# Performance work log

Hardware: AMD Instinct MI355X
Metric: run time of the kernel (lower is better)

The kernel has to match this reference:

```python
import jax, jax.numpy as jnp
import numpy as np

COMMITMENT_COST = 0.25
N, D, K = 131072, 64, 1024


def setup_inputs() -> dict:
    key = jax.random.key(0)
    k1, k2 = jax.random.split(key)
    inputs = jax.random.normal(k1, (N, D), dtype=jnp.float32)
    # torch init: uniform(-1/K, 1/K)
    weight = jax.random.uniform(k2, (K, D), dtype=jnp.float32,
                                minval=-1.0 / K, maxval=1.0 / K)
    return {"inputs": inputs, "weight": weight}


def reference(inputs, weight):
    x2 = jnp.sum(inputs * inputs, axis=1, keepdims=True)          # [N, 1]
    e2 = jnp.sum(weight * weight, axis=1)                          # [K]
    distances = x2 + e2 - 2.0 * jnp.matmul(inputs, weight.T)       # [N, K]
    encoding_indices = jnp.argmin(distances, axis=1)               # [N]
    # scatter one-hot + matmul in the original == direct gather
    quantized = jnp.take(weight, encoding_indices, axis=0)         # [N, D]
    e_latent_loss = jnp.mean((jax.lax.stop_gradient(quantized) - inputs) ** 2)
    q_latent_loss = jnp.mean((quantized - jax.lax.stop_gradient(inputs)) ** 2)
    loss = q_latent_loss + COMMITMENT_COST * e_latent_loss
    # straight-through estimator
    quantized_st = inputs + jax.lax.stop_gradient(quantized - inputs)
    return (quantized_st, loss, encoding_indices)
```

## Files before the change

### kernel.cpp

```cpp
#include <hip/hip_runtime.h>


#define NROWS 131072
#define DIM 64
#define KCODES 1024
#define MARGIN 5e-5f
#define X2_GUARD 120.0f
#define LOSS_SCALE (1.25f / ((float)NROWS * (float)DIM))
#define PADID (1 << 20)

typedef short bf16x8 __attribute__((ext_vector_type(8)));
typedef float f32x4 __attribute__((ext_vector_type(4)));

__device__ __forceinline__ short f2bf(float f) {
    unsigned u = __float_as_uint(f);
    u += 0x7FFF + ((u >> 16) & 1);
    return (short)(u >> 16);
}
__device__ __forceinline__ float bf2f(short h) {
    return __uint_as_float(((unsigned)(unsigned short)h) << 16);
}

__global__ __launch_bounds__(256) void prep_w(const float* __restrict__ w,
                                              float* __restrict__ e2,
                                              short* __restrict__ w_hi,
                                              short* __restrict__ w_lo,
                                              float* __restrict__ out_loss,
                                              unsigned* __restrict__ flag_cnt) {
    int k = blockIdx.x * blockDim.x + threadIdx.x;
    if (k == 0) { *out_loss = 0.0f; *flag_cnt = 0u; }
    if (k >= KCODES) return;
    const float* wk = w + (size_t)k * DIM;
    float r[DIM];
#pragma unroll
    for (int i = 0; i < DIM / 4; ++i) *(float4*)&r[4 * i] = *(const float4*)(wk + 4 * i);
    float s = 0.f;
#pragma unroll
    for (int d = 0; d < DIM; ++d) s = fmaf(r[d], r[d], s);
    e2[k] = s;

    const int t = k >> 5, ct = (k >> 4) & 1, m = k & 15;
#pragma unroll
    for (int kc = 0; kc < 2; ++kc)
#pragma unroll
        for (int q = 0; q < 4; ++q) {
            bf16x8 hv, lv;
#pragma unroll
            for (int j = 0; j < 8; ++j) {
                float f = -2.0f * r[kc * 32 + q * 8 + j];
                short h = f2bf(f);
                hv[j] = h;
                lv[j] = f2bf(f - bf2f(h));
            }
            size_t fo = ((size_t)(((t * 2 + ct) * 2 + kc) * 4 + q) * 16 + m) * 8;
            *(bf16x8*)(w_hi + fo) = hv;
            *(bf16x8*)(w_lo + fo) = lv;
        }
}

#define MINPAIR(av, ai, bv, bi)                                   \
    { bool tk_ = (bv < av) || (bv == av && bi < ai);              \
      av = tk_ ? bv : av; ai = tk_ ? bi : ai; }
#define CEX(xv, xi, yv, yi)                                       \
    { bool tk_ = (yv < xv) || (yv == xv && yi < xi);              \
      float tv_ = xv; int ti_ = xi;                               \
      xv = tk_ ? yv : xv; xi = tk_ ? yi : xi;                     \
      yv = tk_ ? tv_ : yv; yi = tk_ ? ti_ : yi; }

__global__ __launch_bounds__(256, 3) void vq_main(
        const float* __restrict__ x, const float* __restrict__ w,
        const float* __restrict__ e2,
        const short* __restrict__ w_hi, const short* __restrict__ w_lo,
        float* __restrict__ out_q, float* __restrict__ out_loss,
        float* __restrict__ out_idx,
        unsigned* __restrict__ flag_cnt, unsigned* __restrict__ flag_list) {
    const int tid = threadIdx.x;
    const int lane = tid & 63;
    const int wv = tid >> 6;
    const int m = lane & 15;
    const int q = lane >> 4;
    const int block_row0 = blockIdx.x * 128;
    const int wave_row0 = block_row0 + wv * 32;

    __shared__ int sidx[128];
    __shared__ int scnd[128][2];
    __shared__ unsigned char sflg[128];
    __shared__ float red[4];

    float xa[2][2][8];
#pragma unroll
    for (int rt = 0; rt < 2; ++rt) {
        const float* xr = x + (size_t)(wave_row0 + rt * 16 + m) * DIM + q * 8;
        *(float4*)&xa[rt][0][0] = *(const float4*)(xr);
        *(float4*)&xa[rt][0][4] = *(const float4*)(xr + 4);
        *(float4*)&xa[rt][1][0] = *(const float4*)(xr + 32);
        *(float4*)&xa[rt][1][4] = *(const float4*)(xr + 36);
    }
    bf16x8 ah[2][2], al[2][2];
#pragma unroll
    for (int rt = 0; rt < 2; ++rt)
#pragma unroll
        for (int c = 0; c < 2; ++c)
#pragma unroll
            for (int j = 0; j < 8; ++j) {
                float f = xa[rt][c][j];
                short h = f2bf(f);
                ah[rt][c][j] = h;
                al[rt][c][j] = f2bf(f - bf2f(h));
            }

    float best[2][4], sec[2][4];
    int bidx[2][4], sbix[2][4];
#pragma unroll
    for (int rt = 0; rt < 2; ++rt)
#pragma unroll
        for (int r = 0; r < 4; ++r) {
            best[rt][r] = 3.4e38f;
            sec[rt][r] = 3.4e38f;
            bidx[rt][r] = PADID;
            sbix[rt][r] = PADID;
        }

    const short* ph = w_hi + q * 128 + m * 8;
    const short* pl = w_lo + q * 128 + m * 8;
    const float* pe = e2 + m;

    for (int t = 0; t < KCODES / 32; ++t) {
        bf16x8 bh[2][2], bl[2][2];
#pragma unroll
        for (int ct = 0; ct < 2; ++ct)
#pragma unroll
            for (int kc = 0; kc < 2; ++kc) {
                int off = t * 2048 + (ct * 2 + kc) * 512;
                bh[ct][kc] = *(const bf16x8*)(ph + off);
                bl[ct][kc] = *(const bf16x8*)(pl + off);
            }
        float e2c0 = pe[t * 32];
        float e2c1 = pe[t * 32 + 16];

#pragma unroll
        for (int rt = 0; rt < 2; ++rt)
#pragma unroll
            for (int ct = 0; ct < 2; ++ct) {
                float ei = ct ? e2c1 : e2c0;
                f32x4 a = {ei, ei, ei, ei};
                a = __builtin_amdgcn_mfma_f32_16x16x32_bf16(al[rt][0], bh[ct][0], a, 0, 0, 0);
                a = __builtin_amdgcn_mfma_f32_16x16x32_bf16(ah[rt][0], bl[ct][0], a, 0, 0, 0);
                a = __builtin_amdgcn_mfma_f32_16x16x32_bf16(ah[rt][0], bh[ct][0], a, 0, 0, 0);
                a = __builtin_amdgcn_mfma_f32_16x16x32_bf16(al[rt][1], bh[ct][1], a, 0, 0, 0);
                a = __builtin_amdgcn_mfma_f32_16x16x32_bf16(ah[rt][1], bl[ct][1], a, 0, 0, 0);
                a = __builtin_amdgcn_mfma_f32_16x16x32_bf16(ah[rt][1], bh[ct][1], a, 0, 0, 0);
                int id = t * 32 + ct * 16 + m;
#pragma unroll
                for (int r = 0; r < 4; ++r) {
                    float g = a[r];
                    bool ltb = g < best[rt][r];
                    bool lts = g < sec[rt][r];
                    float nsec = ltb ? best[rt][r] : (lts ? g : sec[rt][r]);
                    int nsid = ltb ? bidx[rt][r] : (lts ? id : sbix[rt][r]);
                    best[rt][r] = ltb ? g : best[rt][r];
                    bidx[rt][r] = ltb ? id : bidx[rt][r];
                    sec[rt][r] = nsec;
                    sbix[rt][r] = nsid;
                }
            }
    }

    if (m == 0) {  }
#pragma unroll
    for (int rt = 0; rt < 2; ++rt)
#pragma unroll
        for (int r = 0; r < 4; ++r) {
            float v0 = best[rt][r], v1 = sec[rt][r], v2 = 3.4e38f, v3 = 3.4e38f;
            int j0 = bidx[rt][r], j1 = sbix[rt][r], j2 = PADID, j3 = PADID;
#pragma unroll
            for (int off = 1; off < 16; off <<= 1) {
                float b0 = __shfl_xor(v0, off, 64);
                float b1 = __shfl_xor(v1, off, 64);
                float b2 = __shfl_xor(v2, off, 64);
                float b3 = __shfl_xor(v3, off, 64);
                int k0 = __shfl_xor(j0, off, 64);
                int k1 = __shfl_xor(j1, off, 64);
                int k2 = __shfl_xor(j2, off, 64);
                int k3 = __shfl_xor(j3, off, 64);
                MINPAIR(v0, j0, b3, k3);
                MINPAIR(v1, j1, b2, k2);
                MINPAIR(v2, j2, b1, k1);
                MINPAIR(v3, j3, b0, k0);
                CEX(v0, j0, v2, j2);
                CEX(v1, j1, v3, j3);
                CEX(v0, j0, v1, j1);
                CEX(v2, j2, v3, j3);
            }
            if (m == 0) {
                bool w1 = v1 < v0 + MARGIN;
                bool w2 = v2 < v0 + MARGIN;
                bool w3 = v3 < v0 + MARGIN;
                bool samem = (w1 && ((j0 & 15) == (j1 & 15))) ||
                             (w2 && (((j0 & 15) == (j2 & 15)) ||
                                     ((j1 & 15) == (j2 & 15))));
                int meta;
                if (w3 || samem) meta = 3;
                else if (w2) meta = 2;
                else if (w1) meta = 1;
                else meta = 0;
                int lr = wv * 32 + rt * 16 + q * 4 + r;
                sidx[lr] = j0;
                scnd[lr][0] = j1;
                scnd[lr][1] = j2;
                sflg[lr] = (unsigned char)meta;
                if (meta == 3) {
                    unsigned p = atomicAdd(flag_cnt, 1u);
                    flag_list[p] = (unsigned)(block_row0 + lr);
                }
            }
        }
    __syncthreads();

    float lsum = 0.f;
    const int rl = tid >> 2, part = tid & 3;
#pragma unroll
    for (int p = 0; p < 2; ++p) {
        int lr = p * 64 + rl;
        int grow = block_row0 + lr;
        int meta = sflg[lr];
        if (meta == 0) {
            int bi = sidx[lr];
            const float* xs = x + (size_t)grow * DIM + part * 16;
            const float* ws = w + (size_t)bi * DIM + part * 16;
            float* os = out_q + (size_t)grow * DIM + part * 16;
#pragma unroll
            for (int i = 0; i < 4; ++i) {
                float4 xv = *(const float4*)(xs + 4 * i);
                float4 wv4 = *(const float4*)(ws + 4 * i);
                float d0 = wv4.x - xv.x, d1 = wv4.y - xv.y;
                float d2 = wv4.z - xv.z, d3 = wv4.w - xv.w;
                lsum = fmaf(d0, d0, lsum);
                lsum = fmaf(d1, d1, lsum);
                lsum = fmaf(d2, d2, lsum);
                lsum = fmaf(d3, d3, lsum);
                float4 o = {xv.x + d0, xv.y + d1, xv.z + d2, xv.w + d3};
                *(float4*)(os + 4 * i) = o;
            }
            if (part == 0) out_idx[grow] = (float)bi;
        } else if (meta != 3) {
            int nc = meta + 1;
            int cand = (part == 0) ? sidx[lr]
                     : (part == 1) ? scnd[lr][0] : scnd[lr][1];
            unsigned long long key = ~0ULL;
            float x2v = 0.f;
            if (part < nc) {
                const float* xr = x + (size_t)grow * DIM;
                const float* wr = w + (size_t)cand * DIM;
                float dot = 0.f;
#pragma unroll
                for (int d4 = 0; d4 < 16; ++d4) {
                    float4 xv = *(const float4*)(xr + 4 * d4);
                    float4 wv4 = *(const float4*)(wr + 4 * d4);
                    x2v = fmaf(xv.x, xv.x, x2v);
                    x2v = fmaf(xv.y, xv.y, x2v);
                    x2v = fmaf(xv.z, xv.z, x2v);
                    x2v = fmaf(xv.w, xv.w, x2v);
                    dot = fmaf(xv.x, wv4.x, dot);
                    dot = fmaf(xv.y, wv4.y, dot);
                    dot = fmaf(xv.z, wv4.z, dot);
                    dot = fmaf(xv.w, wv4.w, dot);
                }
                float dist = (x2v + e2[cand]) - 2.0f * dot;
                key = ((unsigned long long)__float_as_uint(dist) << 32) |
                      (unsigned)cand;
            }
            {
                unsigned long long o1 = __shfl_xor(key, 1, 64);
                key = key < o1 ? key : o1;
                unsigned long long o2 = __shfl_xor(key, 2, 64);
                key = key < o2 ? key : o2;
            }
            float x2b = __shfl(x2v, lane & 60, 64);
            if (x2b >= X2_GUARD) {
                if (part == 0) {
                    unsigned pp = atomicAdd(flag_cnt, 1u);
                    flag_list[pp] = (unsigned)grow;
                }
            } else {
                int bi = (int)(unsigned)(key & 0xFFFFFFFFu);
                const float* xs = x + (size_t)grow * DIM + part * 16;
                const float* ws = w + (size_t)bi * DIM + part * 16;
                float* os = out_q + (size_t)grow * DIM + part * 16;
#pragma unroll
                for (int i = 0; i < 4; ++i) {
                    float4 xv = *(const float4*)(xs + 4 * i);
                    float4 wv4 = *(const float4*)(ws + 4 * i);
                    float d0 = wv4.x - xv.x, d1 = wv4.y - xv.y;
                    float d2 = wv4.z - xv.z, d3 = wv4.w - xv.w;
                    lsum = fmaf(d0, d0, lsum);
                    lsum = fmaf(d1, d1, lsum);
                    lsum = fmaf(d2, d2, lsum);
                    lsum = fmaf(d3, d3, lsum);
                    float4 o = {xv.x + d0, xv.y + d1, xv.z + d2, xv.w + d3};
                    *(float4*)(os + 4 * i) = o;
                }
                if (part == 0) out_idx[grow] = (float)bi;
            }
        }
    }

    for (int off = 32; off > 0; off >>= 1) lsum += __shfl_down(lsum, off, 64);
    if ((tid & 63) == 0) red[tid >> 6] = lsum;
    __syncthreads();
    if (tid == 0) {
        float s = (red[0] + red[1]) + (red[2] + red[3]);
        atomicAdd(out_loss, s * LOSS_SCALE);
    }
}

#define CH 16
__global__ __launch_bounds__(256) void vq_cleanup(
        const float* __restrict__ x, const float* __restrict__ w,
        const float* __restrict__ e2,
        const unsigned* __restrict__ flag_cnt,
        const unsigned* __restrict__ flag_list,
        float* __restrict__ out_q, float* __restrict__ out_loss,
        float* __restrict__ out_idx) {
    __shared__ float xs[CH][68];
    __shared__ float wt[128][68];
    __shared__ float sx2[CH];
    const int tid = threadIdx.x;
    const int rowsub = tid >> 4;
    const int kslot = tid & 15;
    const unsigned cnt = *flag_cnt;

    for (unsigned base = blockIdx.x * CH; base < cnt; base += gridDim.x * CH) {
        const int nrows = (int)min((unsigned)CH, cnt - base);
        __syncthreads();
        {
            int rr = tid >> 4, sg = tid & 15;
            if (rr < nrows) {
                unsigned grow = flag_list[base + rr];
                *(float4*)&xs[rr][sg * 4] =
                    *(const float4*)(x + (size_t)grow * DIM + sg * 4);
            }
        }
        __syncthreads();
        if (tid < nrows) {
            float s = 0.f;
#pragma unroll
            for (int d = 0; d < DIM; ++d) s = fmaf(xs[tid][d], xs[tid][d], s);
            sx2[tid] = s;
        }

        unsigned long long kmin = ~0ULL;
        for (int tile = 0; tile < KCODES / 128; ++tile) {
            __syncthreads();
#pragma unroll
            for (int i = 0; i < 8; ++i) {
                int f = tid + i * 256;
                int code = f >> 4, sg = f & 15;
                *(float4*)&wt[code][sg * 4] =
                    *(const float4*)(w + (size_t)(tile * 128 + code) * DIM + sg * 4);
            }
            __syncthreads();
            if (rowsub < nrows) {
#pragma unroll
                for (int j = 0; j < 8; ++j) {
                    int cl = j * 16 + kslot;
                    int code = tile * 128 + cl;
                    float dot = 0.f;
#pragma unroll
                    for (int d4 = 0; d4 < 16; ++d4) {
                        float4 wv4 = *(const float4*)&wt[cl][d4 * 4];
                        float4 xv4 = *(const float4*)&xs[rowsub][d4 * 4];
                        dot = fmaf(wv4.x, xv4.x, dot);
                        dot = fmaf(wv4.y, xv4.y, dot);
                        dot = fmaf(wv4.z, xv4.z, dot);
                        dot = fmaf(wv4.w, xv4.w, dot);
                    }
                    float dist = (sx2[rowsub] + e2[code]) - 2.0f * dot;
                    unsigned long long key =
                        ((unsigned long long)__float_as_uint(dist) << 32) |
                        (unsigned)code;
                    kmin = kmin < key ? kmin : key;
                }
            }
        }
#pragma unroll
        for (int off = 1; off < 16; off <<= 1) {
            unsigned long long o = __shfl_xor(kmin, off, 64);
            kmin = kmin < o ? kmin : o;
        }
        if (rowsub < nrows) {
            int bi = (int)(unsigned)(kmin & 0xFFFFFFFFu);
            unsigned grow = flag_list[base + rowsub];
            float4 x4 = *(float4*)&xs[rowsub][kslot * 4];
            float4 w4 = *(const float4*)(w + (size_t)bi * DIM + kslot * 4);
            float d0 = w4.x - x4.x, d1 = w4.y - x4.y;
            float d2 = w4.z - x4.z, d3 = w4.w - x4.w;
            float ls = 0.f;
            ls = fmaf(d0, d0, ls);
            ls = fmaf(d1, d1, ls);
            ls = fmaf(d2, d2, ls);
            ls = fmaf(d3, d3, ls);
            float4 o = {x4.x + d0, x4.y + d1, x4.z + d2, x4.w + d3};
            *(float4*)(out_q + (size_t)grow * DIM + kslot * 4) = o;
            if (kslot == 0) out_idx[grow] = (float)bi;
#pragma unroll
            for (int off = 1; off < 16; off <<= 1)
                ls += __shfl_xor(ls, off, 64);
            if (kslot == 0) atomicAdd(out_loss, ls * LOSS_SCALE);
        }
    }
}

extern "C" void kernel_launch(void* const* d_in, const int* in_sizes, int n_in,
                              void* d_out, int out_size, void* d_ws, size_t ws_size,
                              hipStream_t stream) {
    const float* x = (const float*)d_in[0];
    const float* w = (const float*)d_in[1];

    float* out_q    = (float*)d_out;
    float* out_loss = (float*)d_out + (size_t)NROWS * DIM;
    float* out_idx  = out_loss + 1;

    float* e2 = (float*)d_ws;
    short* w_hi = (short*)(e2 + KCODES);
    short* w_lo = w_hi + (size_t)KCODES * DIM;
    unsigned* cnt = (unsigned*)(w_lo + (size_t)KCODES * DIM);
    unsigned* list = cnt + 1;

    prep_w<<<(KCODES + 255) / 256, 256, 0, stream>>>(w, e2, w_hi, w_lo,
                                                     out_loss, cnt);
    vq_main<<<NROWS / 128, 256, 0, stream>>>(x, w, e2, w_hi, w_lo,
                                             out_q, out_loss, out_idx, cnt, list);
    vq_cleanup<<<256, 256, 0, stream>>>(x, w, e2, cnt, list,
                                        out_q, out_loss, out_idx);
}
```

Before: 202.6 us.

## Fuse fallback exact-search into main kernel using per-block shared flag list

```diff
diff --git a/kernel.cpp b/kernel.cpp
--- a/kernel.cpp
+++ b/kernel.cpp
@@ -25,10 +25,9 @@
                                               float* __restrict__ e2,
                                               short* __restrict__ w_hi,
                                               short* __restrict__ w_lo,
-                                              float* __restrict__ out_loss,
-                                              unsigned* __restrict__ flag_cnt) {
+                                              float* __restrict__ out_loss) {
     int k = blockIdx.x * blockDim.x + threadIdx.x;
-    if (k == 0) { *out_loss = 0.0f; *flag_cnt = 0u; }
+    if (k == 0) *out_loss = 0.0f;
     if (k >= KCODES) return;
     const float* wk = w + (size_t)k * DIM;
     float r[DIM];
@@ -72,8 +71,7 @@
         const float* __restrict__ e2,
         const short* __restrict__ w_hi, const short* __restrict__ w_lo,
         float* __restrict__ out_q, float* __restrict__ out_loss,
-        float* __restrict__ out_idx,
-        unsigned* __restrict__ flag_cnt, unsigned* __restrict__ flag_list) {
+        float* __restrict__ out_idx) {
     const int tid = threadIdx.x;
     const int lane = tid & 63;
     const int wv = tid >> 6;
@@ -86,6 +84,10 @@
     __shared__ int scnd[128][2];
     __shared__ unsigned char sflg[128];
     __shared__ float red[4];
+    __shared__ int hcnt;
+    __shared__ short hlist[128];
+
+    if (tid == 0) hcnt = 0;
 
     float xa[2][2][8];
 #pragma unroll
@@ -120,6 +122,8 @@
             bidx[rt][r] = PADID;
             sbix[rt][r] = PADID;
         }
+
+    __syncthreads();
 
     const short* ph = w_hi + q * 128 + m * 8;
     const short* pl = w_lo + q * 128 + m * 8;
@@ -166,7 +170,6 @@
             }
     }
 
-    if (m == 0) {  }
 #pragma unroll
     for (int rt = 0; rt < 2; ++rt)
 #pragma unroll
@@ -210,8 +213,8 @@
                 scnd[lr][1] = j2;
                 sflg[lr] = (unsigned char)meta;
                 if (meta == 3) {
-                    unsigned p = atomicAdd(flag_cnt, 1u);
-                    flag_list[p] = (unsigned)(block_row0 + lr);
+                    int p = atomicAdd(&hcnt, 1);
+                    hlist[p] = (short)lr;
                 }
             }
         }
@@ -279,8 +282,8 @@
             float x2b = __shfl(x2v, lane & 60, 64);
             if (x2b >= X2_GUARD) {
                 if (part == 0) {
-                    unsigned pp = atomicAdd(flag_cnt, 1u);
-                    flag_list[pp] = (unsigned)grow;
+                    int pp = atomicAdd(&hcnt, 1);
+                    hlist[pp] = (short)lr;
                 }
             } else {
                 int bi = (int)(unsigned)(key & 0xFFFFFFFFu);
@@ -312,102 +315,66 @@
         float s = (red[0] + red[1]) + (red[2] + red[3]);
         atomicAdd(out_loss, s * LOSS_SCALE);
     }
-}
-
-#define CH 16
-__global__ __launch_bounds__(256) void vq_cleanup(
-        const float* __restrict__ x, const float* __restrict__ w,
-        const float* __restrict__ e2,
-        const unsigned* __restrict__ flag_cnt,
-        const unsigned* __restrict__ flag_list,
-        float* __restrict__ out_q, float* __restrict__ out_loss,
-        float* __restrict__ out_idx) {
-    __shared__ float xs[CH][68];
-    __shared__ float wt[128][68];
-    __shared__ float sx2[CH];
-    const int tid = threadIdx.x;
-    const int rowsub = tid >> 4;
-    const int kslot = tid & 15;
-    const unsigned cnt = *flag_cnt;
-
-    for (unsigned base = blockIdx.x * CH; base < cnt; base += gridDim.x * CH) {
-        const int nrows = (int)min((unsigned)CH, cnt - base);
-        __syncthreads();
-        {
-            int rr = tid >> 4, sg = tid & 15;
-            if (rr < nrows) {
-                unsigned grow = flag_list[base + rr];
-                *(float4*)&xs[rr][sg * 4] =
-                    *(const float4*)(x + (size_t)grow * DIM + sg * 4);
-            }
-        }
-        __syncthreads();
-        if (tid < nrows) {
-            float s = 0.f;
-#pragma unroll
-            for (int d = 0; d < DIM; ++d) s = fmaf(xs[tid][d], xs[tid][d], s);
-            sx2[tid] = s;
-        }
-
+
+    const int nh = hcnt;
+    for (int h = wv; h < nh; h += 4) {
+        const int lr = hlist[h];
+        const int grow = block_row0 + lr;
+        const float* xr = x + (size_t)grow * DIM;
+        float4 xf[16];
+#pragma unroll
+        for (int i = 0; i < 16; ++i) xf[i] = *(const float4*)(xr + 4 * i);
+        float x2 = 0.f;
+#pragma unroll
+        for (int i = 0; i < 16; ++i) {
+            x2 = fmaf(xf[i].x, xf[i].x, x2);
+            x2 = fmaf(xf[i].y, xf[i].y, x2);
+            x2 = fmaf(xf[i].z, xf[i].z, x2);
+            x2 = fmaf(xf[i].w, xf[i].w, x2);
+        }
         unsigned long long kmin = ~0ULL;
-        for (int tile = 0; tile < KCODES / 128; ++tile) {
-            __syncthreads();
-#pragma unroll
-            for (int i = 0; i < 8; ++i) {
-                int f = tid + i * 256;
-                int code = f >> 4, sg = f & 15;
-                *(float4*)&wt[code][sg * 4] =
-                    *(const float4*)(w + (size_t)(tile * 128 + code) * DIM + sg * 4);
-            }
-            __syncthreads();
-            if (rowsub < nrows) {
-#pragma unroll
-                for (int j = 0; j < 8; ++j) {
-                    int cl = j * 16 + kslot;
-                    int code = tile * 128 + cl;
-                    float dot = 0.f;
-#pragma unroll
-                    for (int d4 = 0; d4 < 16; ++d4) {
-                        float4 wv4 = *(const float4*)&wt[cl][d4 * 4];
-                        float4 xv4 = *(const float4*)&xs[rowsub][d4 * 4];
-                        dot = fmaf(wv4.x, xv4.x, dot);
-                        dot = fmaf(wv4.y, xv4.y, dot);
-                        dot = fmaf(wv4.z, xv4.z, dot);
-                        dot = fmaf(wv4.w, xv4.w, dot);
-                    }
-                    float dist = (sx2[rowsub] + e2[code]) - 2.0f * dot;
-                    unsigned long long key =
-                        ((unsigned long long)__float_as_uint(dist) << 32) |
-                        (unsigned)code;
-                    kmin = kmin < key ? kmin : key;
-                }
-            }
-        }
-#pragma unroll
-        for (int off = 1; off < 16; off <<= 1) {
+        for (int jj = 0; jj < 16; ++jj) {
+            int code = jj * 64 + lane;
+            const float* wr = w + (size_t)code * DIM;
+            float dot = 0.f;
+#pragma unroll
+            for (int d4 = 0; d4 < 16; ++d4) {
+                float4 wv4 = *(const float4*)(wr + 4 * d4);
+                dot = fmaf(wv4.x, xf[d4].x, dot);
+                dot = fmaf(wv4.y, xf[d4].y, dot);
+                dot = fmaf(wv4.z, xf[d4].z, dot);
+                dot = fmaf(wv4.w, xf[d4].w, dot);
+            }
+            float dist = (x2 + e2[code]) - 2.0f * dot;
+            unsigned long long key =
+                ((unsigned long long)__float_as_uint(dist) << 32) |
+                (unsigned)code;
+            kmin = kmin < key ? kmin : key;
+        }
+#pragma unroll
+        for (int off = 1; off < 64; off <<= 1) {
             unsigned long long o = __shfl_xor(kmin, off, 64);
             kmin = kmin < o ? kmin : o;
         }
-        if (rowsub < nrows) {
-            int bi = (int)(unsigned)(kmin & 0xFFFFFFFFu);
-            unsigned grow = flag_list[base + rowsub];
-            float4 x4 = *(float4*)&xs[rowsub][kslot * 4];
-            float4 w4 = *(const float4*)(w + (size_t)bi * DIM + kslot * 4);
+        int bi = (int)(unsigned)(kmin & 0xFFFFFFFFu);
+        float ls = 0.f;
+        if (lane < 16) {
+            float4 x4 = *(const float4*)(xr + 4 * lane);
+            float4 w4 = *(const float4*)(w + (size_t)bi * DIM + 4 * lane);
             float d0 = w4.x - x4.x, d1 = w4.y - x4.y;
             float d2 = w4.z - x4.z, d3 = w4.w - x4.w;
-            float ls = 0.f;
             ls = fmaf(d0, d0, ls);
             ls = fmaf(d1, d1, ls);
             ls = fmaf(d2, d2, ls);
             ls = fmaf(d3, d3, ls);
             float4 o = {x4.x + d0, x4.y + d1, x4.z + d2, x4.w + d3};
-            *(float4*)(out_q + (size_t)grow * DIM + kslot * 4) = o;
-            if (kslot == 0) out_idx[grow] = (float)bi;
-#pragma unroll
-            for (int off = 1; off < 16; off <<= 1)
-                ls += __shfl_xor(ls, off, 64);
-            if (kslot == 0) atomicAdd(out_loss, ls * LOSS_SCALE);
-        }
+            *(float4*)(out_q + (size_t)grow * DIM + 4 * lane) = o;
+            if (lane == 0) out_idx[grow] = (float)bi;
+        }
+#pragma unroll
+        for (int off = 1; off < 16; off <<= 1)
+            ls += __shfl_xor(ls, off, 64);
+        if (lane == 0) atomicAdd(out_loss, ls * LOSS_SCALE);
     }
 }
 
@@ -424,13 +391,8 @@
     float* e2 = (float*)d_ws;
     short* w_hi = (short*)(e2 + KCODES);
     short* w_lo = w_hi + (size_t)KCODES * DIM;
-    unsigned* cnt = (unsigned*)(w_lo + (size_t)KCODES * DIM);
-    unsigned* list = cnt + 1;
-
-    prep_w<<<(KCODES + 255) / 256, 256, 0, stream>>>(w, e2, w_hi, w_lo,
-                                                     out_loss, cnt);
+
+    prep_w<<<(KCODES + 255) / 256, 256, 0, stream>>>(w, e2, w_hi, w_lo, out_loss);
     vq_main<<<NROWS / 128, 256, 0, stream>>>(x, w, e2, w_hi, w_lo,
-                                             out_q, out_loss, out_idx, cnt, list);
-    vq_cleanup<<<256, 256, 0, stream>>>(x, w, e2, cnt, list,
-                                        out_q, out_loss, out_idx);
-}
+                                             out_q, out_loss, out_idx);
+}
```

After: 179.9 us. 1.13x faster.

## Fuse flagged-row exact cleanup into main VQ kernel using shared-memory lists

Applied to the files above, without the earlier changes.

```diff
diff --git a/kernel.cpp b/kernel.cpp
--- a/kernel.cpp
+++ b/kernel.cpp
@@ -25,10 +25,9 @@
                                               float* __restrict__ e2,
                                               short* __restrict__ w_hi,
                                               short* __restrict__ w_lo,
-                                              float* __restrict__ out_loss,
-                                              unsigned* __restrict__ flag_cnt) {
+                                              float* __restrict__ out_loss) {
     int k = blockIdx.x * blockDim.x + threadIdx.x;
-    if (k == 0) { *out_loss = 0.0f; *flag_cnt = 0u; }
+    if (k == 0) *out_loss = 0.0f;
     if (k >= KCODES) return;
     const float* wk = w + (size_t)k * DIM;
     float r[DIM];
@@ -72,8 +71,7 @@
         const float* __restrict__ e2,
         const short* __restrict__ w_hi, const short* __restrict__ w_lo,
         float* __restrict__ out_q, float* __restrict__ out_loss,
-        float* __restrict__ out_idx,
-        unsigned* __restrict__ flag_cnt, unsigned* __restrict__ flag_list) {
+        float* __restrict__ out_idx) {
     const int tid = threadIdx.x;
     const int lane = tid & 63;
     const int wv = tid >> 6;
@@ -86,6 +84,13 @@
     __shared__ int scnd[128][2];
     __shared__ unsigned char sflg[128];
     __shared__ float red[4];
+    __shared__ int hcnt;
+    __shared__ short hlist[128];
+    __shared__ float txs[16][68];
+    __shared__ float twt[128][68];
+    __shared__ float tsx2[16];
+
+    if (tid == 0) hcnt = 0;
 
     float xa[2][2][8];
 #pragma unroll
@@ -120,6 +125,8 @@
             bidx[rt][r] = PADID;
             sbix[rt][r] = PADID;
         }
+
+    __syncthreads();
 
     const short* ph = w_hi + q * 128 + m * 8;
     const short* pl = w_lo + q * 128 + m * 8;
@@ -166,7 +173,6 @@
             }
     }
 
-    if (m == 0) {  }
 #pragma unroll
     for (int rt = 0; rt < 2; ++rt)
 #pragma unroll
@@ -210,8 +216,8 @@
                 scnd[lr][1] = j2;
                 sflg[lr] = (unsigned char)meta;
                 if (meta == 3) {
-                    unsigned p = atomicAdd(flag_cnt, 1u);
-                    flag_list[p] = (unsigned)(block_row0 + lr);
+                    int p = atomicAdd(&hcnt, 1);
+                    hlist[p] = (short)lr;
                 }
             }
         }
@@ -279,8 +285,8 @@
             float x2b = __shfl(x2v, lane & 60, 64);
             if (x2b >= X2_GUARD) {
                 if (part == 0) {
-                    unsigned pp = atomicAdd(flag_cnt, 1u);
-                    flag_list[pp] = (unsigned)grow;
+                    int pp = atomicAdd(&hcnt, 1);
+                    hlist[pp] = (short)lr;
                 }
             } else {
                 int bi = (int)(unsigned)(key & 0xFFFFFFFFu);
@@ -312,32 +318,18 @@
         float s = (red[0] + red[1]) + (red[2] + red[3]);
         atomicAdd(out_loss, s * LOSS_SCALE);
     }
-}
-
-#define CH 16
-__global__ __launch_bounds__(256) void vq_cleanup(
-        const float* __restrict__ x, const float* __restrict__ w,
-        const float* __restrict__ e2,
-        const unsigned* __restrict__ flag_cnt,
-        const unsigned* __restrict__ flag_list,
-        float* __restrict__ out_q, float* __restrict__ out_loss,
-        float* __restrict__ out_idx) {
-    __shared__ float xs[CH][68];
-    __shared__ float wt[128][68];
-    __shared__ float sx2[CH];
-    const int tid = threadIdx.x;
+
+    const int nh = hcnt;
     const int rowsub = tid >> 4;
     const int kslot = tid & 15;
-    const unsigned cnt = *flag_cnt;
-
-    for (unsigned base = blockIdx.x * CH; base < cnt; base += gridDim.x * CH) {
-        const int nrows = (int)min((unsigned)CH, cnt - base);
+    for (int base = 0; base < nh; base += 16) {
+        const int nrows = min(16, nh - base);
         __syncthreads();
         {
             int rr = tid >> 4, sg = tid & 15;
             if (rr < nrows) {
-                unsigned grow = flag_list[base + rr];
-                *(float4*)&xs[rr][sg * 4] =
+                int grow = block_row0 + hlist[base + rr];
+                *(float4*)&txs[rr][sg * 4] =
                     *(const float4*)(x + (size_t)grow * DIM + sg * 4);
             }
         }
@@ -345,8 +337,8 @@
         if (tid < nrows) {
             float s = 0.f;
 #pragma unroll
-            for (int d = 0; d < DIM; ++d) s = fmaf(xs[tid][d], xs[tid][d], s);
-            sx2[tid] = s;
+            for (int d = 0; d < DIM; ++d) s = fmaf(txs[tid][d], txs[tid][d], s);
+            tsx2[tid] = s;
         }
 
         unsigned long long kmin = ~0ULL;
@@ -356,7 +348,7 @@
             for (int i = 0; i < 8; ++i) {
                 int f = tid + i * 256;
                 int code = f >> 4, sg = f & 15;
-                *(float4*)&wt[code][sg * 4] =
+                *(float4*)&twt[code][sg * 4] =
                     *(const float4*)(w + (size_t)(tile * 128 + code) * DIM + sg * 4);
             }
             __syncthreads();
@@ -368,14 +360,14 @@
                     float dot = 0.f;
 #pragma unroll
                     for (int d4 = 0; d4 < 16; ++d4) {
-                        float4 wv4 = *(const float4*)&wt[cl][d4 * 4];
-                        float4 xv4 = *(const float4*)&xs[rowsub][d4 * 4];
+                        float4 wv4 = *(const float4*)&twt[cl][d4 * 4];
+                        float4 xv4 = *(const float4*)&txs[rowsub][d4 * 4];
                         dot = fmaf(wv4.x, xv4.x, dot);
                         dot = fmaf(wv4.y, xv4.y, dot);
                         dot = fmaf(wv4.z, xv4.z, dot);
                         dot = fmaf(wv4.w, xv4.w, dot);
                     }
-                    float dist = (sx2[rowsub] + e2[code]) - 2.0f * dot;
+                    float dist = (tsx2[rowsub] + e2[code]) - 2.0f * dot;
                     unsigned long long key =
                         ((unsigned long long)__float_as_uint(dist) << 32) |
                         (unsigned)code;
@@ -390,8 +382,8 @@
         }
         if (rowsub < nrows) {
             int bi = (int)(unsigned)(kmin & 0xFFFFFFFFu);
-            unsigned grow = flag_list[base + rowsub];
-            float4 x4 = *(float4*)&xs[rowsub][kslot * 4];
+            int grow = block_row0 + hlist[base + rowsub];
+            float4 x4 = *(float4*)&txs[rowsub][kslot * 4];
             float4 w4 = *(const float4*)(w + (size_t)bi * DIM + kslot * 4);
             float d0 = w4.x - x4.x, d1 = w4.y - x4.y;
             float d2 = w4.z - x4.z, d3 = w4.w - x4.w;
@@ -424,13 +416,8 @@
     float* e2 = (float*)d_ws;
     short* w_hi = (short*)(e2 + KCODES);
     short* w_lo = w_hi + (size_t)KCODES * DIM;
-    unsigned* cnt = (unsigned*)(w_lo + (size_t)KCODES * DIM);
-    unsigned* list = cnt + 1;
-
-    prep_w<<<(KCODES + 255) / 256, 256, 0, stream>>>(w, e2, w_hi, w_lo,
-                                                     out_loss, cnt);
+
+    prep_w<<<(KCODES + 255) / 256, 256, 0, stream>>>(w, e2, w_hi, w_lo, out_loss);
     vq_main<<<NROWS / 128, 256, 0, stream>>>(x, w, e2, w_hi, w_lo,
-                                             out_q, out_loss, out_idx, cnt, list);
-    vq_cleanup<<<256, 256, 0, stream>>>(x, w, e2, cnt, list,
-                                        out_q, out_loss, out_idx);
+                                             out_q, out_loss, out_idx);
 }
```

After: 217.4 us. +7.3%, slower.
